# Kernel optimization log

Hardware: AMD Instinct MI355X
Metric: run time of the kernel (lower is better)

## Reference

```python
import jax, jax.numpy as jnp
import numpy as np

D_MODEL = 1024
NUM_HEADS = 16
D_HEAD = D_MODEL // NUM_HEADS


def setup_inputs() -> dict:
    key = jax.random.key(0)
    kx, kq, kk, kv, ko = jax.random.split(key, 5)
    scale = 1.0 / np.sqrt(D_MODEL)
    X = jax.random.normal(kx, (4, 2048, D_MODEL), dtype=jnp.float32)
    # nn.Linear weights stored as [out, in]; we keep that convention.
    W_Q = jax.random.uniform(kq, (D_MODEL, D_MODEL), jnp.float32, -scale, scale)
    W_K = jax.random.uniform(kk, (D_MODEL, D_MODEL), jnp.float32, -scale, scale)
    W_V = jax.random.uniform(kv, (D_MODEL, D_MODEL), jnp.float32, -scale, scale)
    W_O = jax.random.uniform(ko, (D_MODEL, D_MODEL), jnp.float32, -scale, scale)
    return {"X": X, "W_Q": W_Q, "W_K": W_K, "W_V": W_V, "W_O": W_O}


def reference(X, W_Q, W_K, W_V, W_O):
    B, S, D = X.shape
    H, Dh = NUM_HEADS, D_HEAD
    # projections (Linear: x @ W.T)
    Q = (X @ W_Q.T).reshape(B, S, H, Dh).transpose(0, 2, 1, 3)  # [B,H,S,Dh]
    K = (X @ W_K.T).reshape(B, S, H, Dh).transpose(0, 2, 1, 3)
    V = (X @ W_V.T).reshape(B, S, H, Dh).transpose(0, 2, 1, 3)
    scores = jnp.einsum('bhqd,bhkd->bhqk', Q, K) / jnp.sqrt(jnp.float32(Dh))
    causal = jnp.tril(jnp.ones((S, S), dtype=bool))  # True = keep
    scores = jnp.where(causal, scores, -jnp.inf)
    attn = jax.nn.softmax(scores, axis=-1)
    out = jnp.einsum('bhqk,bhkd->bhqd', attn, V)  # [B,H,S,Dh]
    out = out.transpose(0, 2, 1, 3).reshape(B, S, D)
    return out @ W_O.T
```

## Files before the change

kernel.cpp:

```cpp
#include <hip/hip_runtime.h>

#define S_LEN 2048
#define NH 16
#define DH 64
#define DM 1024
#define M_TOK 8192
#define SZX ((size_t)M_TOK * DM)
#define SZW ((size_t)DM * DM)

typedef unsigned short u16;
typedef unsigned int u32;
typedef __attribute__((ext_vector_type(8))) short bf16x8;
typedef __attribute__((ext_vector_type(4))) float f32x4;

__device__ __forceinline__ u16 f2bf(float f) {
  union { float f; u32 u; } v; v.f = f;
  return (u16)((v.u + 0x8000u) >> 16);
}
__device__ __forceinline__ u32 pack_bf2(float x, float y) {
  union { float f; u32 u; } a, b; a.f = x; b.f = y;
  return __builtin_amdgcn_perm(b.u + 0x8000u, a.u + 0x8000u, 0x07060302u);
}
__device__ __forceinline__ float fast_exp2(float x) {
  float r; asm("v_exp_f32 %0, %1" : "=v"(r) : "v"(x)); return r;
}
__device__ __forceinline__ void gload16(const u16* g, u16* l) {
  __builtin_amdgcn_global_load_lds((const __attribute__((address_space(1))) void*)g,
                                   (__attribute__((address_space(3))) void*)l,
                                   16, 0, 0);
}

#define QSCALE 0.18033688f

__global__ __launch_bounds__(256) void cast_f32_bf16(const float* __restrict__ src,
                                                     u16* __restrict__ dst, int n) {
  const int i = (blockIdx.x * 256 + threadIdx.x) * 8;
  if (i >= n) return;
  const float4 a = *(const float4*)(src + i);
  const float4 b = *(const float4*)(src + i + 4);
  uint4 r;
  r.x = pack_bf2(a.x, a.y); r.y = pack_bf2(a.z, a.w);
  r.z = pack_bf2(b.x, b.y); r.w = pack_bf2(b.z, b.w);
  *(uint4*)(dst + i) = r;
}

__global__ __launch_bounds__(256) void cast_w4(const float* __restrict__ q,
                                               const float* __restrict__ k,
                                               const float* __restrict__ v,
                                               const float* __restrict__ o,
                                               u16* __restrict__ dst) {
  const int i = (blockIdx.x * 256 + threadIdx.x) * 8;
  const int region = i >> 20;
  const float* src = (region == 0) ? q : (region == 1) ? k : (region == 2) ? v : o;
  const int local = i & ((1 << 20) - 1);
  const float4 a = *(const float4*)(src + local);
  const float4 b = *(const float4*)(src + local + 4);
  uint4 r;
  r.x = pack_bf2(a.x, a.y); r.y = pack_bf2(a.z, a.w);
  r.z = pack_bf2(b.x, b.y); r.w = pack_bf2(b.z, b.w);
  *(uint4*)(dst + i) = r;
}

template<int MODE>
__global__ __launch_bounds__(256) void gemm128(const u16* __restrict__ A,
                                               const u16* __restrict__ Bw,
                                               void* __restrict__ Cv) {
  __shared__ __align__(16) u16 As[128 * 64];
  __shared__ __align__(16) u16 Bs[128 * 64];
  const int tid = threadIdx.x;
  const int lane = tid & 63;
  const int wave = tid >> 6;
  const int col = lane & 15, quad = lane >> 4;
  const int wm = (wave & 1) * 64, wn = (wave >> 1) * 64;
  const int m_blk = blockIdx.x * 128, n_blk = blockIdx.y * 128;

  const int srow = tid >> 3;
  const int skg = (tid & 7) ^ (srow & 7);
  const u16* Ag = A + (size_t)(m_blk + srow) * DM + skg * 8;
  const u16* Bg = Bw + (size_t)(n_blk + srow) * DM + skg * 8;

  f32x4 acc[4][4];
#pragma unroll
  for (int i = 0; i < 4; ++i)
#pragma unroll
    for (int j = 0; j < 4; ++j) acc[i][j] = (f32x4){0.f, 0.f, 0.f, 0.f};

  const int c0 = (quad ^ (col & 7)) * 8;
  const int c1 = c0 ^ 32;

  for (int k0 = 0; k0 < DM; k0 += 64) {
#pragma unroll
    for (int i = 0; i < 4; ++i) {
      gload16(Ag + (size_t)(32 * i) * DM + k0, &As[tid * 8 + i * 2048]);
      gload16(Bg + (size_t)(32 * i) * DM + k0, &Bs[tid * 8 + i * 2048]);
    }
    __syncthreads();
    bf16x8 af[4], bf[4];
#pragma unroll
    for (int i = 0; i < 4; ++i)
      af[i] = *(const bf16x8*)&As[(wm + i * 16 + col) * 64 + c0];
#pragma unroll
    for (int j = 0; j < 4; ++j)
      bf[j] = *(const bf16x8*)&Bs[(wn + j * 16 + col) * 64 + c0];
#pragma unroll
    for (int i = 0; i < 4; ++i)
#pragma unroll
      for (int j = 0; j < 4; ++j)
        acc[i][j] = __builtin_amdgcn_mfma_f32_16x16x32_bf16(af[i], bf[j], acc[i][j], 0, 0, 0);
#pragma unroll
    for (int i = 0; i < 4; ++i)
      af[i] = *(const bf16x8*)&As[(wm + i * 16 + col) * 64 + c1];
#pragma unroll
    for (int j = 0; j < 4; ++j)
      bf[j] = *(const bf16x8*)&Bs[(wn + j * 16 + col) * 64 + c1];
#pragma unroll
    for (int i = 0; i < 4; ++i)
#pragma unroll
      for (int j = 0; j < 4; ++j)
        acc[i][j] = __builtin_amdgcn_mfma_f32_16x16x32_bf16(af[i], bf[j], acc[i][j], 0, 0, 0);
    __syncthreads();
  }

#pragma unroll
  for (int i = 0; i < 4; ++i) {
#pragma unroll
    for (int j = 0; j < 4; ++j) {
      const int n = n_blk + wn + j * 16 + col;
      if (MODE == 0) {
        const int which = n >> 10;
        const int nn = n & 1023;
        const int h = nn >> 6, dh = nn & 63;
        u16* dst = (u16*)Cv + (size_t)which * SZX;
        const int m0 = m_blk + wm + i * 16 + quad * 4;
        const int b = m0 >> 11;
        if (which == 2) {
          uint2 pk;
          pk.x = pack_bf2(acc[i][j][0], acc[i][j][1]);
          pk.y = pack_bf2(acc[i][j][2], acc[i][j][3]);
          *(uint2*)&dst[((size_t)((b * NH + h) * DH + dh)) * S_LEN + (m0 & 2047)] = pk;
        } else {
          const float sc = (which == 0) ? QSCALE : 1.0f;
#pragma unroll
          for (int r = 0; r < 4; ++r) {
            const int m = m0 + r, s = m & 2047;
            dst[((size_t)(b * NH + h) * S_LEN + s) * DH + dh] = f2bf(acc[i][j][r] * sc);
          }
        }
      } else {
#pragma unroll
        for (int r = 0; r < 4; ++r) {
          const int m = m_blk + wm + i * 16 + quad * 4 + r;
          ((float*)Cv)[(size_t)m * DM + n] = acc[i][j][r];
        }
      }
    }
  }
}

#define PLD 72

__device__ __forceinline__ void attn_step(const u16* __restrict__ Ks,
                                          const u16* __restrict__ Vs,
                                          u16* __restrict__ Pw,
                                          bf16x8 qf0, bf16x8 qf1,
                                          float& m_i, float& l_i, f32x4* oacc,
                                          int c0, int c1, int col, int quad,
                                          int q_l, bool diag) {
  f32x4 sa[4];
#pragma unroll
  for (int t = 0; t < 4; ++t) {
    const int row = (t * 16 + col) * 64;
    const bf16x8 kf0 = *(const bf16x8*)&Ks[row + c0];
    const bf16x8 kf1 = *(const bf16x8*)&Ks[row + c1];
    f32x4 z = (f32x4){0.f, 0.f, 0.f, 0.f};
    z = __builtin_amdgcn_mfma_f32_16x16x32_bf16(kf0, qf0, z, 0, 0, 0);
    z = __builtin_amdgcn_mfma_f32_16x16x32_bf16(kf1, qf1, z, 0, 0, 0);
    sa[t] = z;
  }
  float mloc = -1e30f;
#pragma unroll
  for (int t = 0; t < 4; ++t)
#pragma unroll
    for (int r = 0; r < 4; ++r) {
      if (diag && (t * 16 + quad * 4 + r) > q_l) sa[t][r] = -1e30f;
      mloc = fmaxf(mloc, sa[t][r]);
    }
  mloc = fmaxf(mloc, __shfl_xor(mloc, 16, 64));
  mloc = fmaxf(mloc, __shfl_xor(mloc, 32, 64));
  const float newm = fmaxf(m_i, mloc);
  float rsum = 0.f;
#pragma unroll
  for (int t = 0; t < 4; ++t)
#pragma unroll
    for (int r = 0; r < 4; ++r) { sa[t][r] = fast_exp2(sa[t][r] - newm); rsum += sa[t][r]; }
  rsum += __shfl_xor(rsum, 16, 64);
  rsum += __shfl_xor(rsum, 32, 64);
  const float alpha = fast_exp2(m_i - newm);
  l_i = l_i * alpha + rsum;
  m_i = newm;
#pragma unroll
  for (int t = 0; t < 4; ++t) {
    oacc[t][0] *= alpha; oacc[t][1] *= alpha;
    oacc[t][2] *= alpha; oacc[t][3] *= alpha;
    uint2 pk;
    pk.x = pack_bf2(sa[t][0], sa[t][1]);
    pk.y = pack_bf2(sa[t][2], sa[t][3]);
    *(uint2*)&Pw[col * PLD + t * 16 + quad * 4] = pk;
  }
  asm volatile("s_waitcnt lgkmcnt(0)" ::: "memory");
  const bf16x8 pf0 = *(const bf16x8*)&Pw[col * PLD + quad * 8];
  const bf16x8 pf1 = *(const bf16x8*)&Pw[col * PLD + 32 + quad * 8];
#pragma unroll
  for (int t = 0; t < 4; ++t) {
    const int row = (t * 16 + col) * 64;
    const bf16x8 vf0 = *(const bf16x8*)&Vs[row + c0];
    const bf16x8 vf1 = *(const bf16x8*)&Vs[row + c1];
    oacc[t] = __builtin_amdgcn_mfma_f32_16x16x32_bf16(vf0, pf0, oacc[t], 0, 0, 0);
    oacc[t] = __builtin_amdgcn_mfma_f32_16x16x32_bf16(vf1, pf1, oacc[t], 0, 0, 0);
  }
}

__global__ __launch_bounds__(256) void attn_kernel(const u16* __restrict__ Qg,
                                                   const u16* __restrict__ Kg,
                                                   const u16* __restrict__ Vtg,
                                                   u16* __restrict__ AO) {
  __shared__ __align__(16) u16 Ks[64 * 64];
  __shared__ __align__(16) u16 Vs[64 * 64];
  __shared__ __align__(16) u16 Ps[4][16 * PLD];

  const int qtH = 16 + (int)blockIdx.x;
  const int qtL = 31 - qtH;
  const int bh = blockIdx.y;
  const int tid = threadIdx.x, lane = tid & 63, wave = tid >> 6;
  const int col = lane & 15, quad = lane >> 4;

  const u16* Qb = Qg + (size_t)bh * S_LEN * DH;
  const u16* Kb = Kg + (size_t)bh * S_LEN * DH;
  const u16* Vb = Vtg + (size_t)bh * DH * S_LEN;

  const u16* qrowH = Qb + (size_t)(qtH * 64 + wave * 16 + col) * DH + quad * 8;
  const u16* qrowL = Qb + (size_t)(qtL * 64 + wave * 16 + col) * DH + quad * 8;
  const bf16x8 qH0 = *(const bf16x8*)(qrowH);
  const bf16x8 qH1 = *(const bf16x8*)(qrowH + 32);
  const bf16x8 qL0 = *(const bf16x8*)(qrowL);
  const bf16x8 qL1 = *(const bf16x8*)(qrowL + 32);

  float mH = -1e30f, lH = 0.f, mL = -1e30f, lL = 0.f;
  f32x4 oH[4], oL[4];
#pragma unroll
  for (int t = 0; t < 4; ++t) {
    oH[t] = (f32x4){0.f, 0.f, 0.f, 0.f};
    oL[t] = (f32x4){0.f, 0.f, 0.f, 0.f};
  }

  const int sr0 = tid >> 3;
  const int sk0 = (tid & 7) ^ (sr0 & 7);
  const u16* K0 = Kb + (size_t)sr0 * DH + sk0 * 8;
  const u16* K1 = Kb + (size_t)(sr0 + 32) * DH + sk0 * 8;
  const u16* V0 = Vb + (size_t)sr0 * S_LEN + sk0 * 8;
  const u16* V1 = Vb + (size_t)(sr0 + 32) * S_LEN + sk0 * 8;

  const int c0 = (quad ^ (col & 7)) * 8;
  const int c1 = c0 ^ 32;
  const int q_l = wave * 16 + col;
  u16* Pw = &Ps[wave][0];

  for (int kt = 0; kt <= qtH; ++kt) {
    gload16(K0 + (size_t)kt * 64 * DH, &Ks[tid * 8]);
    gload16(K1 + (size_t)kt * 64 * DH, &Ks[2048 + tid * 8]);
    gload16(V0 + kt * 64, &Vs[tid * 8]);
    gload16(V1 + kt * 64, &Vs[2048 + tid * 8]);
    __syncthreads();

    attn_step(Ks, Vs, Pw, qH0, qH1, mH, lH, oH, c0, c1, col, quad, q_l, kt == qtH);
    if (kt <= qtL)
      attn_step(Ks, Vs, Pw, qL0, qL1, mL, lL, oL, c0, c1, col, quad, q_l, kt == qtL);

    __syncthreads();
  }

  const int b = bh >> 4, h = bh & 15;
  {
    const float inv = __builtin_amdgcn_rcpf(lH);
    const size_t base = (size_t)(b * S_LEN + qtH * 64 + q_l) * DM + h * DH;
#pragma unroll
    for (int t = 0; t < 4; ++t) {
      uint2 pk;
      pk.x = pack_bf2(oH[t][0] * inv, oH[t][1] * inv);
      pk.y = pack_bf2(oH[t][2] * inv, oH[t][3] * inv);
      *(uint2*)&AO[base + t * 16 + quad * 4] = pk;
    }
  }
  {
    const float inv = __builtin_amdgcn_rcpf(lL);
    const size_t base = (size_t)(b * S_LEN + qtL * 64 + q_l) * DM + h * DH;
#pragma unroll
    for (int t = 0; t < 4; ++t) {
      uint2 pk;
      pk.x = pack_bf2(oL[t][0] * inv, oL[t][1] * inv);
      pk.y = pack_bf2(oL[t][2] * inv, oL[t][3] * inv);
      *(uint2*)&AO[base + t * 16 + quad * 4] = pk;
    }
  }
}

extern "C" void kernel_launch(void* const* d_in, const int* in_sizes, int n_in,
                              void* d_out, int out_size, void* d_ws, size_t ws_size,
                              hipStream_t stream) {
  const float* X  = (const float*)d_in[0];
  const float* Wq = (const float*)d_in[1];
  const float* Wk = (const float*)d_in[2];
  const float* Wv = (const float*)d_in[3];
  const float* Wo = (const float*)d_in[4];

  u16* Xb   = (u16*)d_ws;
  u16* Wqkv = Xb + SZX;
  u16* Wob  = Wqkv + 3 * SZW;
  u16* Qb   = Wob + SZW;
  u16* Kb   = Qb + SZX;
  u16* VT   = Kb + SZX;
  u16* AO   = Xb;

  cast_f32_bf16<<<(int)(SZX / 8 / 256), 256, 0, stream>>>(X, Xb, (int)SZX);
  cast_w4<<<(int)(4 * SZW / 8 / 256), 256, 0, stream>>>(Wq, Wk, Wv, Wo, Wqkv);

  gemm128<0><<<dim3(M_TOK / 128, 3 * DM / 128), 256, 0, stream>>>(Xb, Wqkv, Qb);

  attn_kernel<<<dim3(16, 4 * NH), 256, 0, stream>>>(Qb, Kb, VT, AO);

  gemm128<1><<<dim3(M_TOK / 128, DM / 128), 256, 0, stream>>>(AO, Wob, d_out);
}
```

Measured before the change: 268.2 us.

## Double-buffer K/V tiles in attention, swizzle P scratch, defer row-sum reduction

Makes the K/V shared-memory tiles double-buffered so the global-to-LDS load of the next tile is issued before computing the current one, and drops one barrier per iteration. Replaces the padded P scratch layout with an XOR-swizzled 64-wide layout to avoid bank conflicts without padding. Moves the cross-lane reduction of the softmax row sum out of the loop to the epilogue, since alpha rescaling is uniform across lanes. This uses more shared memory per block, which can lower occupancy.

```diff
diff --git a/kernel.cpp b/kernel.cpp
--- a/kernel.cpp
+++ b/kernel.cpp
@@ -157,21 +157,20 @@
   }
 }
 
-#define PLD 72
-
-__device__ __forceinline__ void attn_step(const u16* __restrict__ Ks,
-                                          const u16* __restrict__ Vs,
+__device__ __forceinline__ void attn_step(const u16* __restrict__ Ksb,
+                                          const u16* __restrict__ Vsb,
                                           u16* __restrict__ Pw,
                                           bf16x8 qf0, bf16x8 qf1,
                                           float& m_i, float& l_i, f32x4* oacc,
                                           int c0, int c1, int col, int quad,
                                           int q_l, bool diag) {
+  const int colc = col & 7;
   f32x4 sa[4];
 #pragma unroll
   for (int t = 0; t < 4; ++t) {
     const int row = (t * 16 + col) * 64;
-    const bf16x8 kf0 = *(const bf16x8*)&Ks[row + c0];
-    const bf16x8 kf1 = *(const bf16x8*)&Ks[row + c1];
+    const bf16x8 kf0 = *(const bf16x8*)&Ksb[row + c0];
+    const bf16x8 kf1 = *(const bf16x8*)&Ksb[row + c1];
     f32x4 z = (f32x4){0.f, 0.f, 0.f, 0.f};
     z = __builtin_amdgcn_mfma_f32_16x16x32_bf16(kf0, qf0, z, 0, 0, 0);
     z = __builtin_amdgcn_mfma_f32_16x16x32_bf16(kf1, qf1, z, 0, 0, 0);
@@ -193,8 +192,6 @@
   for (int t = 0; t < 4; ++t)
 #pragma unroll
     for (int r = 0; r < 4; ++r) { sa[t][r] = fast_exp2(sa[t][r] - newm); rsum += sa[t][r]; }
-  rsum += __shfl_xor(rsum, 16, 64);
-  rsum += __shfl_xor(rsum, 32, 64);
   const float alpha = fast_exp2(m_i - newm);
   l_i = l_i * alpha + rsum;
   m_i = newm;
@@ -205,16 +202,17 @@
     uint2 pk;
     pk.x = pack_bf2(sa[t][0], sa[t][1]);
     pk.y = pack_bf2(sa[t][2], sa[t][3]);
-    *(uint2*)&Pw[col * PLD + t * 16 + quad * 4] = pk;
+    const int pg = (((t * 2) + (quad >> 1)) ^ colc) * 8 + (quad & 1) * 4;
+    *(uint2*)&Pw[col * 64 + pg] = pk;
   }
   asm volatile("s_waitcnt lgkmcnt(0)" ::: "memory");
-  const bf16x8 pf0 = *(const bf16x8*)&Pw[col * PLD + quad * 8];
-  const bf16x8 pf1 = *(const bf16x8*)&Pw[col * PLD + 32 + quad * 8];
+  const bf16x8 pf0 = *(const bf16x8*)&Pw[col * 64 + ((quad ^ colc) * 8)];
+  const bf16x8 pf1 = *(const bf16x8*)&Pw[col * 64 + (((4 + quad) ^ colc) * 8)];
 #pragma unroll
   for (int t = 0; t < 4; ++t) {
     const int row = (t * 16 + col) * 64;
-    const bf16x8 vf0 = *(const bf16x8*)&Vs[row + c0];
-    const bf16x8 vf1 = *(const bf16x8*)&Vs[row + c1];
+    const bf16x8 vf0 = *(const bf16x8*)&Vsb[row + c0];
+    const bf16x8 vf1 = *(const bf16x8*)&Vsb[row + c1];
     oacc[t] = __builtin_amdgcn_mfma_f32_16x16x32_bf16(vf0, pf0, oacc[t], 0, 0, 0);
     oacc[t] = __builtin_amdgcn_mfma_f32_16x16x32_bf16(vf1, pf1, oacc[t], 0, 0, 0);
   }
@@ -224,9 +222,9 @@
                                                    const u16* __restrict__ Kg,
                                                    const u16* __restrict__ Vtg,
                                                    u16* __restrict__ AO) {
-  __shared__ __align__(16) u16 Ks[64 * 64];
-  __shared__ __align__(16) u16 Vs[64 * 64];
-  __shared__ __align__(16) u16 Ps[4][16 * PLD];
+  __shared__ __align__(16) u16 Ks[2][64 * 64];
+  __shared__ __align__(16) u16 Vs[2][64 * 64];
+  __shared__ __align__(16) u16 Ps[4][16 * 64];
 
   const int qtH = 16 + (int)blockIdx.x;
   const int qtL = 31 - qtH;
@@ -265,23 +263,34 @@
   const int q_l = wave * 16 + col;
   u16* Pw = &Ps[wave][0];
 
+  gload16(K0, &Ks[0][tid * 8]);
+  gload16(K1, &Ks[0][2048 + tid * 8]);
+  gload16(V0, &Vs[0][tid * 8]);
+  gload16(V1, &Vs[0][2048 + tid * 8]);
+
   for (int kt = 0; kt <= qtH; ++kt) {
-    gload16(K0 + (size_t)kt * 64 * DH, &Ks[tid * 8]);
-    gload16(K1 + (size_t)kt * 64 * DH, &Ks[2048 + tid * 8]);
-    gload16(V0 + kt * 64, &Vs[tid * 8]);
-    gload16(V1 + kt * 64, &Vs[2048 + tid * 8]);
     __syncthreads();
-
-    attn_step(Ks, Vs, Pw, qH0, qH1, mH, lH, oH, c0, c1, col, quad, q_l, kt == qtH);
+    if (kt < qtH) {
+      const int nk = kt + 1;
+      const int nb = nk & 1;
+      gload16(K0 + (size_t)nk * 64 * DH, &Ks[nb][tid * 8]);
+      gload16(K1 + (size_t)nk * 64 * DH, &Ks[nb][2048 + tid * 8]);
+      gload16(V0 + nk * 64, &Vs[nb][tid * 8]);
+      gload16(V1 + nk * 64, &Vs[nb][2048 + tid * 8]);
+    }
+    const u16* Ksb = &Ks[kt & 1][0];
+    const u16* Vsb = &Vs[kt & 1][0];
+
+    attn_step(Ksb, Vsb, Pw, qH0, qH1, mH, lH, oH, c0, c1, col, quad, q_l, kt == qtH);
     if (kt <= qtL)
-      attn_step(Ks, Vs, Pw, qL0, qL1, mL, lL, oL, c0, c1, col, quad, q_l, kt == qtL);
-
-    __syncthreads();
+      attn_step(Ksb, Vsb, Pw, qL0, qL1, mL, lL, oL, c0, c1, col, quad, q_l, kt == qtL);
   }
 
   const int b = bh >> 4, h = bh & 15;
   {
-    const float inv = __builtin_amdgcn_rcpf(lH);
+    float lt = lH + __shfl_xor(lH, 16, 64);
+    lt += __shfl_xor(lt, 32, 64);
+    const float inv = __builtin_amdgcn_rcpf(lt);
     const size_t base = (size_t)(b * S_LEN + qtH * 64 + q_l) * DM + h * DH;
 #pragma unroll
     for (int t = 0; t < 4; ++t) {
@@ -292,7 +301,9 @@
     }
   }
   {
-    const float inv = __builtin_amdgcn_rcpf(lL);
+    float lt = lL + __shfl_xor(lL, 16, 64);
+    lt += __shfl_xor(lt, 32, 64);
+    const float inv = __builtin_amdgcn_rcpf(lt);
     const size_t base = (size_t)(b * S_LEN + qtL * 64 + q_l) * DM + h * DH;
 #pragma unroll
     for (int t = 0; t < 4; ++t) {
```

Measured after the change: 266.1 us. About the same (-0.8%).
